# Kernel optimization log

Measured on AMD Instinct MI355X. Metric: run time of the kernel, lower is better.

Reference implementation:

```python
import jax, jax.numpy as jnp
import numpy as np

ALPHA = 0.5  # self.alpha


def gcn_conv(x, ei, W, b, n_nodes):
    """PyG GCNConv: sym-normalized A+I aggregation of x @ W.T, plus bias."""
    h = x @ W.T  # [N, H]
    sl = jnp.arange(n_nodes)
    row = jnp.concatenate([ei[0], sl])  # sources (+ self loops)
    col = jnp.concatenate([ei[1], sl])  # targets (+ self loops)
    deg = jax.ops.segment_sum(jnp.ones_like(row, dtype=h.dtype), col, num_segments=n_nodes)
    dinv = jnp.where(deg > 0, jax.lax.rsqrt(deg), 0.0)
    norm = dinv[row] * dinv[col]
    msg = norm[:, None] * h[row]
    out = jax.ops.segment_sum(msg, col, num_segments=n_nodes)
    return out + b


def attention(Ws, A, bA):
    """Bilinear cross-view attention over weight matrices Ws [V, K, D].
    attn[i,j] = sum_k (Ws[i,k] @ A @ Ws[j,k] + bias); row-softmax."""
    K = Ws.shape[1]
    T = jnp.einsum('vka,ab->vkb', Ws, A)
    M = jnp.einsum('vkb,wkb->vw', T, Ws) + K * bA[0]
    return jax.nn.softmax(M, axis=1)


def cross_rep(x_inner, x_lin, att, alpha):
    # temp_i = alpha * sum_j att[i,j] * x_lin[j]; res = (1-alpha) + x_inner + elu(temp)
    cross = alpha * jnp.einsum('vw,wnh->vnh', att, x_lin)
    return (1.0 - alpha) + x_inner + jax.nn.elu(cross)


def setup_inputs() -> dict:
    key = jax.random.key(0)
    ks = jax.random.split(key, 20)
    N, D, H, V, E, Eev = 50000, 128, 128, 3, 800000, 100000
    s_d = 1.0 / np.sqrt(D)
    s_h = 1.0 / np.sqrt(H)
    s_c = 1.0 / np.sqrt(V * H)
    inp = {
        'x': jax.random.normal(ks[0], (N, D), dtype=jnp.float32),
        'W1': jax.random.normal(ks[1], (V, H, D), dtype=jnp.float32) * s_d,
        'b1': jnp.zeros((V, H), dtype=jnp.float32),
        'W2': jax.random.normal(ks[2], (V, H, H), dtype=jnp.float32) * s_h,
        'b2': jnp.zeros((V, H), dtype=jnp.float32),
        'A1': jax.random.normal(ks[3], (D, D), dtype=jnp.float32) * s_d,
        'bA1': jnp.zeros((1,), dtype=jnp.float32),
        'A2': jax.random.normal(ks[4], (H, H), dtype=jnp.float32) * s_h,
        'bA2': jnp.zeros((1,), dtype=jnp.float32),
        'Wc1': jax.random.normal(ks[5], (H, V * H), dtype=jnp.float32) * s_c,
        'bc1': jnp.zeros((H,), dtype=jnp.float32),
        'Wc2': jax.random.normal(ks[6], (H, V * H), dtype=jnp.float32) * s_c,
        'bc2': jnp.zeros((H,), dtype=jnp.float32),
        'edge_index': jax.random.randint(ks[7], (V, 2, E), 0, N, dtype=jnp.int64),
        'edges': jax.random.randint(ks[8], (V, Eev, 2), 0, N, dtype=jnp.int64),
        'edges_neg': jax.random.randint(ks[9], (V, Eev, 2), 0, N, dtype=jnp.int64),
    }
    return inp


def reference(x, W1, b1, W2, b2, A1, bA1, A2, bA2, Wc1, bc1, Wc2, bc2,
              edge_index, edges, edges_neg):
    N = x.shape[0]
    V = W1.shape[0]

    # layer 1: per-view GCNConv + ELU (dropout = identity in eval)
    x1 = jnp.stack([jax.nn.elu(gcn_conv(x, edge_index[v], W1[v], b1[v], N))
                    for v in range(V)])  # [V, N, H]
    xlin1 = jnp.einsum('nd,vhd->vnh', x, W1)  # conv.lin(x) per view
    att1 = attention(W1, A1, bA1)
    xr1 = cross_rep(x1, xlin1, att1, ALPHA)

    # combine 1: concat views along feature dim, linear + ELU
    emb = xr1.transpose(1, 0, 2).reshape(N, -1)  # [N, V*H]
    xc = jax.nn.elu(emb @ Wc1.T + bc1)  # [N, H]

    # layer 2: per-view GCNConv (no activation before cross rep)
    x2 = jnp.stack([gcn_conv(xc, edge_index[v], W2[v], b2[v], N)
                    for v in range(V)])
    xlin2 = jnp.einsum('nd,vhd->vnh', xc, W2)
    att2 = attention(W2, A2, bA2)
    xr2 = cross_rep(x2, xlin2, att2, ALPHA)

    # per-view edge scoring: dot products on pos then neg edges, concatenated
    def score(xv, e_pos, e_neg):
        p = jnp.sum(xv[e_pos[:, 0]] * xv[e_pos[:, 1]], axis=-1)
        n = jnp.sum(xv[e_neg[:, 0]] * xv[e_neg[:, 1]], axis=-1)
        return jnp.concatenate([p, n])

    results = jax.vmap(score)(xr2, edges, edges_neg)  # [V, 2*Eev]
    return results
```

## Files before the change

### kernel.cpp

```cpp
#include <hip/hip_runtime.h>
#include <hip/hip_bf16.h>


#define THREADS 256
#define BCH 8192

typedef __bf16 bf16x8 __attribute__((ext_vector_type(8)));
typedef float f32x4 __attribute__((ext_vector_type(4)));
typedef unsigned short us8 __attribute__((ext_vector_type(8)));
typedef unsigned short us4 __attribute__((ext_vector_type(4)));

__device__ __forceinline__ float eluf(float x) {
    return x > 0.f ? x : expm1f(x);
}

__device__ __forceinline__ unsigned short f2bf(float f) {
    unsigned u = __builtin_bit_cast(unsigned, f);
    u += 0x7FFF + ((u >> 16) & 1);
    return (unsigned short)(u >> 16);
}
__device__ __forceinline__ float bf2f(unsigned short s) {
    unsigned u = ((unsigned)s) << 16;
    return __builtin_bit_cast(float, u);
}

__global__ __launch_bounds__(THREADS) void init_int_kernel(int* p, int n) {
    int i = blockIdx.x * THREADS + threadIdx.x;
    if (i < n) p[i] = 0;
}

__global__ __launch_bounds__(THREADS) void dinv_kernel(
    const int* __restrict__ cnt, float* __restrict__ dinv, int VN) {
    int i = blockIdx.x * THREADS + threadIdx.x;
    if (i < VN) dinv[i] = rsqrtf((float)(cnt[i] + 1));
}


__global__ __launch_bounds__(THREADS) void bucket_count_kernel(
    const int* __restrict__ ei, int* __restrict__ bcnt, int N, int E, int VE) {
    __shared__ int h[160];
    for (int i = threadIdx.x; i < 160; i += THREADS) h[i] = 0;
    __syncthreads();
    int base = blockIdx.x * BCH;
    for (int k = 0; k < BCH; k += THREADS) {
        int t = base + k + threadIdx.x;
        if (t < VE) {
            int v = (t >= E) + (t >= 2 * E);
            int e = t - v * E;
            int col = ei[(size_t)v * 2 * E + E + e];
            atomicAdd(&h[(v * N + col) >> 10], 1);
        }
    }
    __syncthreads();
    for (int i = threadIdx.x; i < 160; i += THREADS)
        if (h[i]) atomicAdd(&bcnt[i], h[i]);
}

__global__ __launch_bounds__(THREADS) void bucket_scan_kernel(
    const int* __restrict__ bcnt, int* __restrict__ bstart, int* __restrict__ bofs, int nb) {
    __shared__ int sh[THREADS];
    int t = threadIdx.x;
    int v = (t < nb) ? bcnt[t] : 0;
    sh[t] = v;
    __syncthreads();
    for (int off = 1; off < THREADS; off <<= 1) {
        int u = (t >= off) ? sh[t - off] : 0;
        __syncthreads();
        sh[t] += u;
        __syncthreads();
    }
    int excl = sh[t] - v;
    if (t < nb) { bstart[t] = excl; bofs[t] = excl; }
    if (t == nb - 1) bstart[nb] = sh[t];
}

__global__ __launch_bounds__(THREADS) void bucket_scatter_kernel(
    const int* __restrict__ ei, int* __restrict__ bofs,
    int* __restrict__ coo_g, int* __restrict__ coo_r, int N, int E, int VE) {
    __shared__ int h[160];
    __shared__ int cur[160];
    for (int i = threadIdx.x; i < 160; i += THREADS) h[i] = 0;
    __syncthreads();
    int base = blockIdx.x * BCH;
    for (int k = 0; k < BCH; k += THREADS) {
        int t = base + k + threadIdx.x;
        if (t < VE) {
            int v = (t >= E) + (t >= 2 * E);
            int e = t - v * E;
            int col = ei[(size_t)v * 2 * E + E + e];
            atomicAdd(&h[(v * N + col) >> 10], 1);
        }
    }
    __syncthreads();
    if (threadIdx.x < 160 && h[threadIdx.x])
        cur[threadIdx.x] = atomicAdd(&bofs[threadIdx.x], h[threadIdx.x]);
    __syncthreads();
    for (int k = 0; k < BCH; k += THREADS) {
        int t = base + k + threadIdx.x;
        if (t < VE) {
            int v = (t >= E) + (t >= 2 * E);
            int e = t - v * E;
            const int* eiv = ei + (size_t)v * 2 * E;
            int row = eiv[e], col = eiv[E + e];
            int g = v * N + col;
            int pos = atomicAdd(&cur[g >> 10], 1);
            coo_g[pos] = g;
            coo_r[pos] = row;
        }
    }
}

__global__ __launch_bounds__(THREADS) void bucket_hist_kernel(
    const int* __restrict__ coo_g, const int* __restrict__ bstart,
    int* __restrict__ cnt, int VN) {
    __shared__ int h[1024];
    for (int i = threadIdx.x; i < 1024; i += THREADS) h[i] = 0;
    __syncthreads();
    int b = blockIdx.x;
    int s = bstart[b], e = bstart[b + 1];
    for (int i = s + threadIdx.x; i < e; i += THREADS)
        atomicAdd(&h[coo_g[i] & 1023], 1);
    __syncthreads();
    int g0 = b << 10;
    for (int i = threadIdx.x; i < 1024; i += THREADS)
        if (g0 + i < VN) cnt[g0 + i] = h[i];
}

__global__ __launch_bounds__(THREADS) void bucket_fill_kernel(
    const int* __restrict__ coo_g, const int* __restrict__ coo_r,
    const int* __restrict__ bstart, int* __restrict__ ptr,
    int* __restrict__ idx, int VN) {
    __shared__ int p[1024];
    int b = blockIdx.x, g0 = b << 10;
    for (int i = threadIdx.x; i < 1024; i += THREADS)
        p[i] = (g0 + i < VN) ? ptr[g0 + i] : 0;
    __syncthreads();
    int s = bstart[b], e = bstart[b + 1];
    for (int i = s + threadIdx.x; i < e; i += THREADS) {
        int pos = atomicAdd(&p[coo_g[i] & 1023], 1);
        idx[pos] = coo_r[i];
    }
    __syncthreads();
    for (int i = threadIdx.x; i < 1024; i += THREADS)
        if (g0 + i < VN) ptr[g0 + i] = p[i];
}

#define SC_T 256
#define SC_CHUNK 1024

__global__ __launch_bounds__(SC_T) void scan_sum_kernel(
    const int* __restrict__ cnt, int* __restrict__ bsum, int n) {
    __shared__ int red[SC_T];
    int base = blockIdx.x * SC_CHUNK + threadIdx.x * 4;
    int s = 0;
#pragma unroll
    for (int k = 0; k < 4; k++) {
        int i = base + k;
        if (i < n) s += cnt[i];
    }
    red[threadIdx.x] = s;
    __syncthreads();
    for (int st = SC_T / 2; st; st >>= 1) {
        if (threadIdx.x < st) red[threadIdx.x] += red[threadIdx.x + st];
        __syncthreads();
    }
    if (threadIdx.x == 0) bsum[blockIdx.x] = red[0];
}

__global__ __launch_bounds__(SC_T) void scan_top_kernel(int* bsum, int nb) {
    __shared__ int sh[SC_T];
    int t = threadIdx.x;
    int v = (t < nb) ? bsum[t] : 0;
    sh[t] = v;
    __syncthreads();
    for (int off = 1; off < SC_T; off <<= 1) {
        int u = (t >= off) ? sh[t - off] : 0;
        __syncthreads();
        sh[t] += u;
        __syncthreads();
    }
    if (t < nb) bsum[t] = sh[t] - v;
}

__global__ __launch_bounds__(SC_T) void scan_apply_kernel(
    const int* __restrict__ cnt, const int* __restrict__ bsum,
    int* __restrict__ ptr, int n) {
    __shared__ int sh[SC_T];
    int base = blockIdx.x * SC_CHUNK + threadIdx.x * 4;
    int v[4];
    int s = 0;
#pragma unroll
    for (int k = 0; k < 4; k++) {
        int i = base + k;
        v[k] = (i < n) ? cnt[i] : 0;
        s += v[k];
    }
    int tin = s;
    sh[threadIdx.x] = s;
    __syncthreads();
    for (int off = 1; off < SC_T; off <<= 1) {
        int u = (threadIdx.x >= off) ? sh[threadIdx.x - off] : 0;
        __syncthreads();
        sh[threadIdx.x] += u;
        __syncthreads();
    }
    int run = bsum[blockIdx.x] + sh[threadIdx.x] - tin;
#pragma unroll
    for (int k = 0; k < 4; k++) {
        int i = base + k;
        if (i < n) {
            ptr[i] = run;
            run += v[k];
        }
    }
}

template <int SPLIT3>
__global__ __launch_bounds__(256) void gemm_mfma_kernel(
    const float* __restrict__ A, const float* __restrict__ B,
    const float* __restrict__ bias, float* __restrict__ Cf,
    unsigned short* __restrict__ Cbf, const float* __restrict__ dscale,
    int M, int Kb, size_t AV, size_t Bz, size_t Cz) {
    extern __shared__ unsigned short sm[];
    unsigned short* Ahi = sm;
    unsigned short* Bhi = sm + 8192;
    unsigned short* Alo = SPLIT3 ? sm + 16384 : nullptr;
    unsigned short* Blo = SPLIT3 ? sm + 24576 : nullptr;
    int tid = threadIdx.x;
    int z = blockIdx.z;
    int m0 = blockIdx.x * 128;
    const float* Bp = B + (size_t)z * Bz;
    int lane = tid & 63, wid = tid >> 6;
    int wr = wid >> 1, wc = wid & 1;
    int lr = lane & 15, lg = lane >> 4;
    f32x4 acc[4][4] = {};

    for (int k0 = 0; k0 < Kb; k0 += 64) {
        size_t Abase = (size_t)(k0 >> 7) * AV + (k0 & 127);
        for (int i = 0; i < 4; ++i) {
            int ch = tid + i * 256;
            int row = ch >> 3, c8 = (ch & 7) << 3;
            int e = (row * 64 + c8) ^ ((row & 7) << 3);
            float va[8];
            int gm = m0 + row;
            if (gm < M) {
                const float* p = A + Abase + (size_t)gm * 128 + c8;
                *(float4*)(va)     = *(const float4*)(p);
                *(float4*)(va + 4) = *(const float4*)(p + 4);
            } else {
#pragma unroll
                for (int j = 0; j < 8; j++) va[j] = 0.f;
            }
            us8 h8, l8;
#pragma unroll
            for (int j = 0; j < 8; j++) {
                unsigned short h = f2bf(va[j]);
                h8[j] = h;
                if (SPLIT3) l8[j] = f2bf(va[j] - bf2f(h));
            }
            *(us8*)&Ahi[e] = h8;
            if (SPLIT3) *(us8*)&Alo[e] = l8;
            float vb[8];
            const float* q = Bp + (size_t)row * Kb + k0 + c8;
            *(float4*)(vb)     = *(const float4*)(q);
            *(float4*)(vb + 4) = *(const float4*)(q + 4);
#pragma unroll
            for (int j = 0; j < 8; j++) {
                unsigned short h = f2bf(vb[j]);
                h8[j] = h;
                if (SPLIT3) l8[j] = f2bf(vb[j] - bf2f(h));
            }
            *(us8*)&Bhi[e] = h8;
            if (SPLIT3) *(us8*)&Blo[e] = l8;
        }
        __syncthreads();
#pragma unroll
        for (int ks = 0; ks < 2; ++ks) {
            bf16x8 ah[4], al[4], bh[4], bl[4];
#pragma unroll
            for (int m = 0; m < 4; m++) {
                int row = wr * 64 + m * 16 + lr;
                int e = (row * 64 + ks * 32 + lg * 8) ^ ((row & 7) << 3);
                ah[m] = *(const bf16x8*)&Ahi[e];
                if (SPLIT3) al[m] = *(const bf16x8*)&Alo[e];
            }
#pragma unroll
            for (int n = 0; n < 4; n++) {
                int col = wc * 64 + n * 16 + lr;
                int e = (col * 64 + ks * 32 + lg * 8) ^ ((col & 7) << 3);
                bh[n] = *(const bf16x8*)&Bhi[e];
                if (SPLIT3) bl[n] = *(const bf16x8*)&Blo[e];
            }
#pragma unroll
            for (int m = 0; m < 4; m++)
#pragma unroll
                for (int n = 0; n < 4; n++) {
                    acc[m][n] = __builtin_amdgcn_mfma_f32_16x16x32_bf16(ah[m], bh[n], acc[m][n], 0, 0, 0);
                    if (SPLIT3) {
                        acc[m][n] = __builtin_amdgcn_mfma_f32_16x16x32_bf16(ah[m], bl[n], acc[m][n], 0, 0, 0);
                        acc[m][n] = __builtin_amdgcn_mfma_f32_16x16x32_bf16(al[m], bh[n], acc[m][n], 0, 0, 0);
                    }
                }
        }
        __syncthreads();
    }

#pragma unroll
    for (int m = 0; m < 4; m++) {
        int rbase = m0 + wr * 64 + m * 16 + lg * 4;
#pragma unroll
        for (int n = 0; n < 4; n++) {
            int col = wc * 64 + n * 16 + lr;
#pragma unroll
            for (int j = 0; j < 4; j++) {
                int row = rbase + j;
                if (row < M) {
                    float vv = acc[m][n][j];
                    if (Cbf) {
                        float sc = dscale[(size_t)z * M + row];
                        Cbf[(size_t)z * Cz + (size_t)row * 128 + col] = f2bf(vv * sc);
                    } else {
                        Cf[(size_t)z * Cz + (size_t)row * 128 + col] = eluf(vv + bias[col]);
                    }
                }
            }
        }
    }
}

__global__ __launch_bounds__(THREADS) void small_mm_nn_kernel(
    const float* __restrict__ W, const float* __restrict__ A, float* __restrict__ T) {
    int idx = blockIdx.x * THREADS + threadIdx.x;
    if (idx >= 3 * 128 * 128) return;
    int b = idx & 127;
    int vk = idx >> 7;
    const float* w = W + (size_t)vk * 128;
    float s = 0.f;
#pragma unroll 8
    for (int a = 0; a < 128; a++) s += w[a] * A[a * 128 + b];
    T[idx] = s;
}

__global__ __launch_bounds__(THREADS) void att_reduce_kernel(
    const float* __restrict__ T, const float* __restrict__ W,
    const float* __restrict__ bA, float* __restrict__ Mraw) {
    int v = blockIdx.x / 3, w = blockIdx.x % 3;
    const float* tp = T + (size_t)v * 16384;
    const float* wp = W + (size_t)w * 16384;
    float s = 0.f;
    for (int i = threadIdx.x; i < 16384; i += THREADS) s += tp[i] * wp[i];
    __shared__ float red[THREADS];
    red[threadIdx.x] = s;
    __syncthreads();
    for (int st = THREADS / 2; st; st >>= 1) {
        if (threadIdx.x < st) red[threadIdx.x] += red[threadIdx.x + st];
        __syncthreads();
    }
    if (threadIdx.x == 0) Mraw[blockIdx.x] = red[0] + 128.f * bA[0];
}

__global__ void att_softmax_kernel(const float* __restrict__ Mraw, float* __restrict__ att) {
    int v = threadIdx.x;
    if (v >= 3) return;
    float m0 = Mraw[v * 3 + 0], m1 = Mraw[v * 3 + 1], m2 = Mraw[v * 3 + 2];
    float mx = fmaxf(m0, fmaxf(m1, m2));
    float e0 = expf(m0 - mx), e1 = expf(m1 - mx), e2 = expf(m2 - mx);
    float s = e0 + e1 + e2;
    att[v * 3 + 0] = e0 / s;
    att[v * 3 + 1] = e1 / s;
    att[v * 3 + 2] = e2 / s;
}

template <int OUTBF>
__global__ __launch_bounds__(THREADS) void gather_cross_kernel(
    const unsigned short* __restrict__ xs, const float* __restrict__ dinv,
    const int* __restrict__ ptr, const int* __restrict__ idx,
    const float* __restrict__ att, const float* __restrict__ bias,
    float* __restrict__ xrf, unsigned short* __restrict__ xrb,
    int N, int elu_inner) {
    int wv = (blockIdx.x * THREADS + threadIdx.x) >> 6;
    int lane = threadIdx.x & 63;
    int VN = 3 * N;
    if (wv >= VN) return;
    int v = wv / N;
    int n = wv - v * N;
    int vN = v * N;
    int g = lane >> 4, f0 = (lane & 15) * 8;

    float acc[8] = {};
    int s = (wv == 0) ? 0 : ptr[wv - 1];
    int e = ptr[wv];
    int j = s + g;
    for (; j + 4 < e; j += 8) {
        int r0 = idx[j], r1 = idx[j + 4];
        us8 u0 = *(const us8*)(xs + (((size_t)(vN + r0)) << 7) + f0);
        us8 u1 = *(const us8*)(xs + (((size_t)(vN + r1)) << 7) + f0);
#pragma unroll
        for (int i = 0; i < 8; i++) acc[i] += bf2f(u0[i]) + bf2f(u1[i]);
    }
    if (j < e) {
        int r0 = idx[j];
        us8 u0 = *(const us8*)(xs + (((size_t)(vN + r0)) << 7) + f0);
#pragma unroll
        for (int i = 0; i < 8; i++) acc[i] += bf2f(u0[i]);
    }
#pragma unroll
    for (int i = 0; i < 8; i++) {
        acc[i] += __shfl_xor(acc[i], 16);
        acc[i] += __shfl_xor(acc[i], 32);
    }

    if (g == 0) {
        us8 su = *(const us8*)(xs + (((size_t)wv) << 7) + f0);
        float dc = dinv[wv];
        size_t nb = (((size_t)n) << 7) + f0;
        size_t NH = ((size_t)N) << 7;
        us8 c0 = *(const us8*)(xs + nb);
        us8 c1 = *(const us8*)(xs + NH + nb);
        us8 c2 = *(const us8*)(xs + 2 * NH + nb);
        float wa = att[v * 3 + 0] / dinv[n];
        float wb = att[v * 3 + 1] / dinv[N + n];
        float wc = att[v * 3 + 2] / dinv[2 * N + n];
        float4 bb0 = *(const float4*)(bias + v * 128 + f0);
        float4 bb1 = *(const float4*)(bias + v * 128 + f0 + 4);
        float bv[8] = {bb0.x, bb0.y, bb0.z, bb0.w, bb1.x, bb1.y, bb1.z, bb1.w};
        float ov[8];
#pragma unroll
        for (int i = 0; i < 8; i++) {
            float a = dc * (acc[i] + bf2f(su[i])) + bv[i];
            if (elu_inner) a = eluf(a);
            float cr = wa * bf2f(c0[i]) + wb * bf2f(c1[i]) + wc * bf2f(c2[i]);
            ov[i] = 0.5f + a + eluf(0.5f * cr);
        }
        if (OUTBF) {
            us8 o;
#pragma unroll
            for (int i = 0; i < 8; i++) o[i] = f2bf(ov[i]);
            *(us8*)(xrb + (((size_t)wv) << 7) + f0) = o;
        } else {
            float4 o0 = {ov[0], ov[1], ov[2], ov[3]};
            float4 o1 = {ov[4], ov[5], ov[6], ov[7]};
            *(float4*)(xrf + (((size_t)wv) << 7) + f0)     = o0;
            *(float4*)(xrf + (((size_t)wv) << 7) + f0 + 4) = o1;
        }
    }
}

__global__ __launch_bounds__(THREADS) void edge_score_kernel(
    const unsigned short* __restrict__ xr2, const int* __restrict__ edges,
    const int* __restrict__ edges_neg, float* __restrict__ out, int N, int Eev, int V) {
    int half = (blockIdx.x * THREADS + threadIdx.x) >> 5;
    int l32 = threadIdx.x & 31;
    int total = V * 2 * Eev;
    if (half >= total) return;
    int v = half / (2 * Eev);
    int r = half - v * (2 * Eev);
    const int* ep = (r < Eev) ? edges + ((size_t)v * Eev + r) * 2
                              : edges_neg + ((size_t)v * Eev + (r - Eev)) * 2;
    int a = ep[0], b = ep[1];
    const unsigned short* pa = xr2 + (((size_t)v * N + a) << 7) + l32 * 4;
    const unsigned short* pb = xr2 + (((size_t)v * N + b) << 7) + l32 * 4;
    us4 ua = *(const us4*)pa, ub = *(const us4*)pb;
    float s = bf2f(ua[0]) * bf2f(ub[0]) + bf2f(ua[1]) * bf2f(ub[1]) +
              bf2f(ua[2]) * bf2f(ub[2]) + bf2f(ua[3]) * bf2f(ub[3]);
#pragma unroll
    for (int off = 16; off; off >>= 1) s += __shfl_xor(s, off, 32);
    if (l32 == 0) out[half] = s;
}

extern "C" void kernel_launch(void* const* d_in, const int* in_sizes, int n_in,
                              void* d_out, int out_size, void* d_ws, size_t ws_size,
                              hipStream_t stream) {
    const float* x   = (const float*)d_in[0];
    const float* W1  = (const float*)d_in[1];
    const float* b1  = (const float*)d_in[2];
    const float* W2  = (const float*)d_in[3];
    const float* b2  = (const float*)d_in[4];
    const float* A1  = (const float*)d_in[5];
    const float* bA1 = (const float*)d_in[6];
    const float* A2  = (const float*)d_in[7];
    const float* bA2 = (const float*)d_in[8];
    const float* Wc1 = (const float*)d_in[9];
    const float* bc1 = (const float*)d_in[10];
    const int* ei        = (const int*)d_in[13];
    const int* edges     = (const int*)d_in[14];
    const int* edges_neg = (const int*)d_in[15];
    float* out = (float*)d_out;

    const int H = 128, V = 3;
    const int N = in_sizes[0] / H;
    const int E = in_sizes[13] / (V * 2);
    const int Eev = in_sizes[14] / (V * 2);
    const int VNH = V * N * H;
    const int VN = V * N;
    const int VE = V * E;
    const int NB = (VN + 1023) >> 10;

    float* ws   = (float*)d_ws;
    float* agg  = ws;
    float* xc   = agg + VNH;
    float* dinv = xc + (size_t)N * H;
    float* T    = dinv + VN;
    float* Mraw = T + 3 * 128 * 128;
    float* att  = Mraw + 16;
    int* cnt    = (int*)(att + 16);
    int* ptr    = cnt + VN;
    int* bsum   = ptr + VN;
    int* bcnt   = bsum + 256;
    int* bstart = bcnt + 256;
    int* bofs   = bstart + 256;
    int* idx    = bofs + 256;
    int* coo_g  = idx + VE;
    int* coo_r  = coo_g + VE;
    unsigned short* xs = (unsigned short*)(coo_r + VE);
    unsigned short* xr2b = (unsigned short*)agg;
    (void)ws_size; (void)n_in; (void)out_size;

    dim3 blk(THREADS);
    int gVN = (VN + THREADS - 1) / THREADS;
    int gBC = (VE + BCH - 1) / BCH;
    int gGather = (int)(((size_t)VN * 64 + THREADS - 1) / THREADS);
    int nScanB = (VN + SC_CHUNK - 1) / SC_CHUNK;
    dim3 gemmGrid((N + 127) / 128, 1, V);
    dim3 gemmGrid1((N + 127) / 128, 1, 1);
    int gScore = (int)(((size_t)V * 2 * Eev * 32 + THREADS - 1) / THREADS);

    init_int_kernel<<<1, blk, 0, stream>>>(bcnt, 256);
    bucket_count_kernel<<<gBC, blk, 0, stream>>>(ei, bcnt, N, E, VE);
    bucket_scan_kernel<<<1, blk, 0, stream>>>(bcnt, bstart, bofs, NB);
    bucket_scatter_kernel<<<gBC, blk, 0, stream>>>(ei, bofs, coo_g, coo_r, N, E, VE);
    bucket_hist_kernel<<<NB, blk, 0, stream>>>(coo_g, bstart, cnt, VN);
    dinv_kernel<<<gVN, blk, 0, stream>>>(cnt, dinv, VN);
    scan_sum_kernel<<<nScanB, SC_T, 0, stream>>>(cnt, bsum, VN);
    scan_top_kernel<<<1, SC_T, 0, stream>>>(bsum, nScanB);
    scan_apply_kernel<<<nScanB, SC_T, 0, stream>>>(cnt, bsum, ptr, VN);
    bucket_fill_kernel<<<NB, blk, 0, stream>>>(coo_g, coo_r, bstart, ptr, idx, VN);

    gemm_mfma_kernel<0><<<gemmGrid, blk, 32768, stream>>>(
        x, W1, nullptr, nullptr, xs, dinv, N, 128, (size_t)0, (size_t)128 * 128, (size_t)N * 128);
    small_mm_nn_kernel<<<(3 * 128 * 128 + THREADS - 1) / THREADS, blk, 0, stream>>>(W1, A1, T);
    att_reduce_kernel<<<9, blk, 0, stream>>>(T, W1, bA1, Mraw);
    att_softmax_kernel<<<1, 64, 0, stream>>>(Mraw, att);
    gather_cross_kernel<0><<<gGather, blk, 0, stream>>>(xs, dinv, ptr, idx, att, b1, agg, nullptr, N, 1);

    gemm_mfma_kernel<1><<<gemmGrid1, blk, 65536, stream>>>(
        agg, Wc1, bc1, xc, nullptr, nullptr, N, 384, (size_t)N * 128, (size_t)0, (size_t)0);

    gemm_mfma_kernel<0><<<gemmGrid, blk, 32768, stream>>>(
        xc, W2, nullptr, nullptr, xs, dinv, N, 128, (size_t)0, (size_t)128 * 128, (size_t)N * 128);
    small_mm_nn_kernel<<<(3 * 128 * 128 + THREADS - 1) / THREADS, blk, 0, stream>>>(W2, A2, T);
    att_reduce_kernel<<<9, blk, 0, stream>>>(T, W2, bA2, Mraw);
    att_softmax_kernel<<<1, 64, 0, stream>>>(Mraw, att);
    gather_cross_kernel<1><<<gGather, blk, 0, stream>>>(xs, dinv, ptr, idx, att, b2, nullptr, xr2b, N, 0);

    edge_score_kernel<<<gScore, blk, 0, stream>>>(xr2b, edges, edges_neg, out, N, Eev, V);
}
```

Before: 627.2 us.

## Store intermediates in bf16, drop split-bf16 GEMM, batch attention kernels

The layer-1 cross-rep output and the combine-layer output are now stored as bf16, and the combine GEMM uses plain bf16 MFMA instead of the three-pass hi/lo split. This cuts memory traffic and MFMA work. The dinv computation moves into the scan-apply kernel, and the attention kernels for both layers run in single batched launches. The gather loop is unrolled to four rows per step, and edge scoring uses 16 lanes with 8-wide loads. Numerical accuracy drops because the combine GEMM loses its low-order correction terms and the intermediates are rounded to bf16.

```diff
diff --git a/kernel.cpp b/kernel.cpp
--- a/kernel.cpp
+++ b/kernel.cpp
@@ -8,7 +8,6 @@
 typedef __bf16 bf16x8 __attribute__((ext_vector_type(8)));
 typedef float f32x4 __attribute__((ext_vector_type(4)));
 typedef unsigned short us8 __attribute__((ext_vector_type(8)));
-typedef unsigned short us4 __attribute__((ext_vector_type(4)));
 
 __device__ __forceinline__ float eluf(float x) {
     return x > 0.f ? x : expm1f(x);
@@ -27,12 +26,6 @@
 __global__ __launch_bounds__(THREADS) void init_int_kernel(int* p, int n) {
     int i = blockIdx.x * THREADS + threadIdx.x;
     if (i < n) p[i] = 0;
-}
-
-__global__ __launch_bounds__(THREADS) void dinv_kernel(
-    const int* __restrict__ cnt, float* __restrict__ dinv, int VN) {
-    int i = blockIdx.x * THREADS + threadIdx.x;
-    if (i < VN) dinv[i] = rsqrtf((float)(cnt[i] + 1));
 }
 
 
@@ -184,7 +177,7 @@
 
 __global__ __launch_bounds__(SC_T) void scan_apply_kernel(
     const int* __restrict__ cnt, const int* __restrict__ bsum,
-    int* __restrict__ ptr, int n) {
+    int* __restrict__ ptr, float* __restrict__ dinv, int n) {
     __shared__ int sh[SC_T];
     int base = blockIdx.x * SC_CHUNK + threadIdx.x * 4;
     int v[4];
@@ -211,21 +204,19 @@
         if (i < n) {
             ptr[i] = run;
             run += v[k];
-        }
-    }
-}
-
-template <int SPLIT3>
-__global__ __launch_bounds__(256) void gemm_mfma_kernel(
-    const float* __restrict__ A, const float* __restrict__ B,
-    const float* __restrict__ bias, float* __restrict__ Cf,
-    unsigned short* __restrict__ Cbf, const float* __restrict__ dscale,
+            dinv[i] = rsqrtf((float)(v[k] + 1));
+        }
+    }
+}
+
+template <int ABF>
+__global__ __launch_bounds__(256) void gemm_bf16_kernel(
+    const float* __restrict__ Af, const unsigned short* __restrict__ Ab,
+    const float* __restrict__ B, const float* __restrict__ bias,
+    unsigned short* __restrict__ C, const float* __restrict__ dscale,
     int M, int Kb, size_t AV, size_t Bz, size_t Cz) {
-    extern __shared__ unsigned short sm[];
-    unsigned short* Ahi = sm;
-    unsigned short* Bhi = sm + 8192;
-    unsigned short* Alo = SPLIT3 ? sm + 16384 : nullptr;
-    unsigned short* Blo = SPLIT3 ? sm + 24576 : nullptr;
+    __shared__ unsigned short Ah[128 * 64];
+    __shared__ unsigned short Bh[128 * 64];
     int tid = threadIdx.x;
     int z = blockIdx.z;
     int m0 = blockIdx.x * 128;
@@ -241,66 +232,59 @@
             int ch = tid + i * 256;
             int row = ch >> 3, c8 = (ch & 7) << 3;
             int e = (row * 64 + c8) ^ ((row & 7) << 3);
-            float va[8];
             int gm = m0 + row;
-            if (gm < M) {
-                const float* p = A + Abase + (size_t)gm * 128 + c8;
-                *(float4*)(va)     = *(const float4*)(p);
-                *(float4*)(va + 4) = *(const float4*)(p + 4);
+            us8 h8;
+            if (ABF) {
+                if (gm < M) {
+                    h8 = *(const us8*)(Ab + Abase + (size_t)gm * 128 + c8);
+                } else {
+#pragma unroll
+                    for (int j = 0; j < 8; j++) h8[j] = 0;
+                }
             } else {
-#pragma unroll
-                for (int j = 0; j < 8; j++) va[j] = 0.f;
+                float va[8];
+                if (gm < M) {
+                    const float* p = Af + Abase + (size_t)gm * 128 + c8;
+                    *(float4*)(va)     = *(const float4*)(p);
+                    *(float4*)(va + 4) = *(const float4*)(p + 4);
+                } else {
+#pragma unroll
+                    for (int j = 0; j < 8; j++) va[j] = 0.f;
+                }
+#pragma unroll
+                for (int j = 0; j < 8; j++) h8[j] = f2bf(va[j]);
             }
-            us8 h8, l8;
-#pragma unroll
-            for (int j = 0; j < 8; j++) {
-                unsigned short h = f2bf(va[j]);
-                h8[j] = h;
-                if (SPLIT3) l8[j] = f2bf(va[j] - bf2f(h));
-            }
-            *(us8*)&Ahi[e] = h8;
-            if (SPLIT3) *(us8*)&Alo[e] = l8;
+            *(us8*)&Ah[e] = h8;
             float vb[8];
             const float* q = Bp + (size_t)row * Kb + k0 + c8;
             *(float4*)(vb)     = *(const float4*)(q);
             *(float4*)(vb + 4) = *(const float4*)(q + 4);
-#pragma unroll
-            for (int j = 0; j < 8; j++) {
-                unsigned short h = f2bf(vb[j]);
-                h8[j] = h;
-                if (SPLIT3) l8[j] = f2bf(vb[j] - bf2f(h));
-            }
-            *(us8*)&Bhi[e] = h8;
-            if (SPLIT3) *(us8*)&Blo[e] = l8;
+            us8 b8;
+#pragma unroll
+            for (int j = 0; j < 8; j++) b8[j] = f2bf(vb[j]);
+            *(us8*)&Bh[e] = b8;
         }
         __syncthreads();
 #pragma unroll
         for (int ks = 0; ks < 2; ++ks) {
-            bf16x8 ah[4], al[4], bh[4], bl[4];
+            bf16x8 ah[4], bh[4];
 #pragma unroll
             for (int m = 0; m < 4; m++) {
                 int row = wr * 64 + m * 16 + lr;
                 int e = (row * 64 + ks * 32 + lg * 8) ^ ((row & 7) << 3);
-                ah[m] = *(const bf16x8*)&Ahi[e];
-                if (SPLIT3) al[m] = *(const bf16x8*)&Alo[e];
+                ah[m] = *(const bf16x8*)&Ah[e];
             }
 #pragma unroll
             for (int n = 0; n < 4; n++) {
                 int col = wc * 64 + n * 16 + lr;
                 int e = (col * 64 + ks * 32 + lg * 8) ^ ((col & 7) << 3);
-                bh[n] = *(const bf16x8*)&Bhi[e];
-                if (SPLIT3) bl[n] = *(const bf16x8*)&Blo[e];
+                bh[n] = *(const bf16x8*)&Bh[e];
             }
 #pragma unroll
             for (int m = 0; m < 4; m++)
 #pragma unroll
-                for (int n = 0; n < 4; n++) {
+                for (int n = 0; n < 4; n++)
                     acc[m][n] = __builtin_amdgcn_mfma_f32_16x16x32_bf16(ah[m], bh[n], acc[m][n], 0, 0, 0);
-                    if (SPLIT3) {
-                        acc[m][n] = __builtin_amdgcn_mfma_f32_16x16x32_bf16(ah[m], bl[n], acc[m][n], 0, 0, 0);
-                        acc[m][n] = __builtin_amdgcn_mfma_f32_16x16x32_bf16(al[m], bh[n], acc[m][n], 0, 0, 0);
-                    }
-                }
         }
         __syncthreads();
     }
@@ -316,12 +300,9 @@
                 int row = rbase + j;
                 if (row < M) {
                     float vv = acc[m][n][j];
-                    if (Cbf) {
-                        float sc = dscale[(size_t)z * M + row];
-                        Cbf[(size_t)z * Cz + (size_t)row * 128 + col] = f2bf(vv * sc);
-                    } else {
-                        Cf[(size_t)z * Cz + (size_t)row * 128 + col] = eluf(vv + bias[col]);
-                    }
+                    if (bias) vv = eluf(vv + bias[col]);
+                    if (dscale) vv *= dscale[(size_t)z * M + row];
+                    C[(size_t)z * Cz + (size_t)row * 128 + col] = f2bf(vv);
                 }
             }
         }
@@ -329,24 +310,32 @@
 }
 
 __global__ __launch_bounds__(THREADS) void small_mm_nn_kernel(
-    const float* __restrict__ W, const float* __restrict__ A, float* __restrict__ T) {
-    int idx = blockIdx.x * THREADS + threadIdx.x;
-    if (idx >= 3 * 128 * 128) return;
-    int b = idx & 127;
-    int vk = idx >> 7;
-    const float* w = W + (size_t)vk * 128;
+    const float* __restrict__ W1, const float* __restrict__ W2,
+    const float* __restrict__ A1, const float* __restrict__ A2,
+    float* __restrict__ T) {
+    int lin = blockIdx.x * THREADS + threadIdx.x;
+    if (lin >= 2 * 3 * 128 * 128) return;
+    int l = lin / 49152;
+    int rem = lin - l * 49152;
+    int b = rem & 127;
+    int vk = rem >> 7;
+    const float* w = (l ? W2 : W1) + (size_t)vk * 128;
+    const float* A = l ? A2 : A1;
     float s = 0.f;
 #pragma unroll 8
     for (int a = 0; a < 128; a++) s += w[a] * A[a * 128 + b];
-    T[idx] = s;
+    T[lin] = s;
 }
 
 __global__ __launch_bounds__(THREADS) void att_reduce_kernel(
-    const float* __restrict__ T, const float* __restrict__ W,
-    const float* __restrict__ bA, float* __restrict__ Mraw) {
-    int v = blockIdx.x / 3, w = blockIdx.x % 3;
-    const float* tp = T + (size_t)v * 16384;
-    const float* wp = W + (size_t)w * 16384;
+    const float* __restrict__ T, const float* __restrict__ W1,
+    const float* __restrict__ W2, const float* __restrict__ bA1,
+    const float* __restrict__ bA2, float* __restrict__ Mraw) {
+    int l = blockIdx.x / 9;
+    int vw = blockIdx.x - l * 9;
+    int v = vw / 3, w = vw - v * 3;
+    const float* tp = T + (size_t)l * 49152 + (size_t)v * 16384;
+    const float* wp = (l ? W2 : W1) + (size_t)w * 16384;
     float s = 0.f;
     for (int i = threadIdx.x; i < 16384; i += THREADS) s += tp[i] * wp[i];
     __shared__ float red[THREADS];
@@ -356,12 +345,12 @@
         if (threadIdx.x < st) red[threadIdx.x] += red[threadIdx.x + st];
         __syncthreads();
     }
-    if (threadIdx.x == 0) Mraw[blockIdx.x] = red[0] + 128.f * bA[0];
+    if (threadIdx.x == 0) Mraw[blockIdx.x] = red[0] + 128.f * (l ? bA2[0] : bA1[0]);
 }
 
 __global__ void att_softmax_kernel(const float* __restrict__ Mraw, float* __restrict__ att) {
     int v = threadIdx.x;
-    if (v >= 3) return;
+    if (v >= 6) return;
     float m0 = Mraw[v * 3 + 0], m1 = Mraw[v * 3 + 1], m2 = Mraw[v * 3 + 2];
     float mx = fmaxf(m0, fmaxf(m1, m2));
     float e0 = expf(m0 - mx), e1 = expf(m1 - mx), e2 = expf(m2 - mx);
@@ -371,13 +360,11 @@
     att[v * 3 + 2] = e2 / s;
 }
 
-template <int OUTBF>
 __global__ __launch_bounds__(THREADS) void gather_cross_kernel(
     const unsigned short* __restrict__ xs, const float* __restrict__ dinv,
     const int* __restrict__ ptr, const int* __restrict__ idx,
     const float* __restrict__ att, const float* __restrict__ bias,
-    float* __restrict__ xrf, unsigned short* __restrict__ xrb,
-    int N, int elu_inner) {
+    unsigned short* __restrict__ xr, int N, int elu_inner) {
     int wv = (blockIdx.x * THREADS + threadIdx.x) >> 6;
     int lane = threadIdx.x & 63;
     int VN = 3 * N;
@@ -391,14 +378,17 @@
     int s = (wv == 0) ? 0 : ptr[wv - 1];
     int e = ptr[wv];
     int j = s + g;
-    for (; j + 4 < e; j += 8) {
-        int r0 = idx[j], r1 = idx[j + 4];
+    for (; j + 12 < e; j += 16) {
+        int r0 = idx[j], r1 = idx[j + 4], r2 = idx[j + 8], r3 = idx[j + 12];
         us8 u0 = *(const us8*)(xs + (((size_t)(vN + r0)) << 7) + f0);
         us8 u1 = *(const us8*)(xs + (((size_t)(vN + r1)) << 7) + f0);
-#pragma unroll
-        for (int i = 0; i < 8; i++) acc[i] += bf2f(u0[i]) + bf2f(u1[i]);
-    }
-    if (j < e) {
+        us8 u2 = *(const us8*)(xs + (((size_t)(vN + r2)) << 7) + f0);
+        us8 u3 = *(const us8*)(xs + (((size_t)(vN + r3)) << 7) + f0);
+#pragma unroll
+        for (int i = 0; i < 8; i++)
+            acc[i] += (bf2f(u0[i]) + bf2f(u1[i])) + (bf2f(u2[i]) + bf2f(u3[i]));
+    }
+    for (; j < e; j += 4) {
         int r0 = idx[j];
         us8 u0 = *(const us8*)(xs + (((size_t)(vN + r0)) << 7) + f0);
 #pragma unroll
@@ -424,48 +414,41 @@
         float4 bb0 = *(const float4*)(bias + v * 128 + f0);
         float4 bb1 = *(const float4*)(bias + v * 128 + f0 + 4);
         float bv[8] = {bb0.x, bb0.y, bb0.z, bb0.w, bb1.x, bb1.y, bb1.z, bb1.w};
-        float ov[8];
+        us8 o;
 #pragma unroll
         for (int i = 0; i < 8; i++) {
             float a = dc * (acc[i] + bf2f(su[i])) + bv[i];
             if (elu_inner) a = eluf(a);
             float cr = wa * bf2f(c0[i]) + wb * bf2f(c1[i]) + wc * bf2f(c2[i]);
-            ov[i] = 0.5f + a + eluf(0.5f * cr);
-        }
-        if (OUTBF) {
-            us8 o;
-#pragma unroll
-            for (int i = 0; i < 8; i++) o[i] = f2bf(ov[i]);
-            *(us8*)(xrb + (((size_t)wv) << 7) + f0) = o;
-        } else {
-            float4 o0 = {ov[0], ov[1], ov[2], ov[3]};
-            float4 o1 = {ov[4], ov[5], ov[6], ov[7]};
-            *(float4*)(xrf + (((size_t)wv) << 7) + f0)     = o0;
-            *(float4*)(xrf + (((size_t)wv) << 7) + f0 + 4) = o1;
-        }
+            o[i] = f2bf(0.5f + a + eluf(0.5f * cr));
+        }
+        *(us8*)(xr + (((size_t)wv) << 7) + f0) = o;
     }
 }
 
 __global__ __launch_bounds__(THREADS) void edge_score_kernel(
     const unsigned short* __restrict__ xr2, const int* __restrict__ edges,
     const int* __restrict__ edges_neg, float* __restrict__ out, int N, int Eev, int V) {
-    int half = (blockIdx.x * THREADS + threadIdx.x) >> 5;
-    int l32 = threadIdx.x & 31;
+    int q = (blockIdx.x * THREADS + threadIdx.x) >> 4;
+    int l16 = threadIdx.x & 15;
     int total = V * 2 * Eev;
-    if (half >= total) return;
-    int v = half / (2 * Eev);
-    int r = half - v * (2 * Eev);
+    if (q >= total) return;
+    int v = q / (2 * Eev);
+    int r = q - v * (2 * Eev);
     const int* ep = (r < Eev) ? edges + ((size_t)v * Eev + r) * 2
                               : edges_neg + ((size_t)v * Eev + (r - Eev)) * 2;
     int a = ep[0], b = ep[1];
-    const unsigned short* pa = xr2 + (((size_t)v * N + a) << 7) + l32 * 4;
-    const unsigned short* pb = xr2 + (((size_t)v * N + b) << 7) + l32 * 4;
-    us4 ua = *(const us4*)pa, ub = *(const us4*)pb;
-    float s = bf2f(ua[0]) * bf2f(ub[0]) + bf2f(ua[1]) * bf2f(ub[1]) +
-              bf2f(ua[2]) * bf2f(ub[2]) + bf2f(ua[3]) * bf2f(ub[3]);
-#pragma unroll
-    for (int off = 16; off; off >>= 1) s += __shfl_xor(s, off, 32);
-    if (l32 == 0) out[half] = s;
+    const unsigned short* pa = xr2 + (((size_t)v * N + a) << 7) + l16 * 8;
+    const unsigned short* pb = xr2 + (((size_t)v * N + b) << 7) + l16 * 8;
+    us8 ua = *(const us8*)pa, ub = *(const us8*)pb;
+    float s = 0.f;
+#pragma unroll
+    for (int i = 0; i < 8; i++) s += bf2f(ua[i]) * bf2f(ub[i]);
+    s += __shfl_xor(s, 8);
+    s += __shfl_xor(s, 4);
+    s += __shfl_xor(s, 2);
+    s += __shfl_xor(s, 1);
+    if (l16 == 0) out[q] = s;
 }
 
 extern "C" void kernel_launch(void* const* d_in, const int* in_sizes, int n_in,
@@ -497,13 +480,11 @@
     const int NB = (VN + 1023) >> 10;
 
     float* ws   = (float*)d_ws;
-    float* agg  = ws;
-    float* xc   = agg + VNH;
-    float* dinv = xc + (size_t)N * H;
+    float* dinv = ws;
     float* T    = dinv + VN;
-    float* Mraw = T + 3 * 128 * 128;
-    float* att  = Mraw + 16;
-    int* cnt    = (int*)(att + 16);
+    float* Mraw = T + 98304;
+    float* att  = Mraw + 32;
+    int* cnt    = (int*)(att + 32);
     int* ptr    = cnt + VN;
     int* bsum   = ptr + VN;
     int* bcnt   = bsum + 256;
@@ -513,45 +494,42 @@
     int* coo_g  = idx + VE;
     int* coo_r  = coo_g + VE;
     unsigned short* xs = (unsigned short*)(coo_r + VE);
-    unsigned short* xr2b = (unsigned short*)agg;
+    unsigned short* xr = xs + VNH;
+    unsigned short* xc = xr + VNH;
     (void)ws_size; (void)n_in; (void)out_size;
 
     dim3 blk(THREADS);
-    int gVN = (VN + THREADS - 1) / THREADS;
     int gBC = (VE + BCH - 1) / BCH;
     int gGather = (int)(((size_t)VN * 64 + THREADS - 1) / THREADS);
     int nScanB = (VN + SC_CHUNK - 1) / SC_CHUNK;
     dim3 gemmGrid((N + 127) / 128, 1, V);
     dim3 gemmGrid1((N + 127) / 128, 1, 1);
-    int gScore = (int)(((size_t)V * 2 * Eev * 32 + THREADS - 1) / THREADS);
+    int gScore = (int)(((size_t)V * 2 * Eev * 16 + THREADS - 1) / THREADS);
 
     init_int_kernel<<<1, blk, 0, stream>>>(bcnt, 256);
     bucket_count_kernel<<<gBC, blk, 0, stream>>>(ei, bcnt, N, E, VE);
     bucket_scan_kernel<<<1, blk, 0, stream>>>(bcnt, bstart, bofs, NB);
     bucket_scatter_kernel<<<gBC, blk, 0, stream>>>(ei, bofs, coo_g, coo_r, N, E, VE);
     bucket_hist_kernel<<<NB, blk, 0, stream>>>(coo_g, bstart, cnt, VN);
-    dinv_kernel<<<gVN, blk, 0, stream>>>(cnt, dinv, VN);
     scan_sum_kernel<<<nScanB, SC_T, 0, stream>>>(cnt, bsum, VN);
     scan_top_kernel<<<1, SC_T, 0, stream>>>(bsum, nScanB);
-    scan_apply_kernel<<<nScanB, SC_T, 0, stream>>>(cnt, bsum, ptr, VN);
+    scan_apply_kernel<<<nScanB, SC_T, 0, stream>>>(cnt, bsum, ptr, dinv, VN);
     bucket_fill_kernel<<<NB, blk, 0, stream>>>(coo_g, coo_r, bstart, ptr, idx, VN);
 
-    gemm_mfma_kernel<0><<<gemmGrid, blk, 32768, stream>>>(
-        x, W1, nullptr, nullptr, xs, dinv, N, 128, (size_t)0, (size_t)128 * 128, (size_t)N * 128);
-    small_mm_nn_kernel<<<(3 * 128 * 128 + THREADS - 1) / THREADS, blk, 0, stream>>>(W1, A1, T);
-    att_reduce_kernel<<<9, blk, 0, stream>>>(T, W1, bA1, Mraw);
+    small_mm_nn_kernel<<<(2 * 49152 + THREADS - 1) / THREADS, blk, 0, stream>>>(W1, W2, A1, A2, T);
+    att_reduce_kernel<<<18, blk, 0, stream>>>(T, W1, W2, bA1, bA2, Mraw);
     att_softmax_kernel<<<1, 64, 0, stream>>>(Mraw, att);
-    gather_cross_kernel<0><<<gGather, blk, 0, stream>>>(xs, dinv, ptr, idx, att, b1, agg, nullptr, N, 1);
-
-    gemm_mfma_kernel<1><<<gemmGrid1, blk, 65536, stream>>>(
-        agg, Wc1, bc1, xc, nullptr, nullptr, N, 384, (size_t)N * 128, (size_t)0, (size_t)0);
-
-    gemm_mfma_kernel<0><<<gemmGrid, blk, 32768, stream>>>(
-        xc, W2, nullptr, nullptr, xs, dinv, N, 128, (size_t)0, (size_t)128 * 128, (size_t)N * 128);
-    small_mm_nn_kernel<<<(3 * 128 * 128 + THREADS - 1) / THREADS, blk, 0, stream>>>(W2, A2, T);
-    att_reduce_kernel<<<9, blk, 0, stream>>>(T, W2, bA2, Mraw);
-    att_softmax_kernel<<<1, 64, 0, stream>>>(Mraw, att);
-    gather_cross_kernel<1><<<gGather, blk, 0, stream>>>(xs, dinv, ptr, idx, att, b2, nullptr, xr2b, N, 0);
-
-    edge_score_kernel<<<gScore, blk, 0, stream>>>(xr2b, edges, edges_neg, out, N, Eev, V);
-}
+
+    gemm_bf16_kernel<0><<<gemmGrid, blk, 0, stream>>>(
+        x, nullptr, W1, nullptr, xs, dinv, N, 128, (size_t)0, (size_t)128 * 128, (size_t)N * 128);
+    gather_cross_kernel<<<gGather, blk, 0, stream>>>(xs, dinv, ptr, idx, att, b1, xr, N, 1);
+
+    gemm_bf16_kernel<1><<<gemmGrid1, blk, 0, stream>>>(
+        nullptr, xr, Wc1, bc1, xc, nullptr, N, 384, (size_t)N * 128, (size_t)0, (size_t)0);
+
+    gemm_bf16_kernel<1><<<gemmGrid, blk, 0, stream>>>(
+        nullptr, xc, W2, nullptr, xs, dinv, N, 128, (size_t)0, (size_t)128 * 128, (size_t)N * 128);
+    gather_cross_kernel<<<gGather, blk, 0, stream>>>(xs, dinv, ptr, idx, att + 9, b2, xr, N, 0);
+
+    edge_score_kernel<<<gScore, blk, 0, stream>>>(xr, edges, edges_neg, out, N, Eev, V);
+}
```

After: 584.7 us. -6.8%, faster.
